# Kernel tuning notes

Hardware: AMD Instinct MI355X
Metric: run time of the kernel (lower is better)

## Reference

```python
import jax, jax.numpy as jnp
import numpy as np

B, N, NY = 2, 4096, 4096
ENC_DIM, DEC_DIM, H = 768, 512, 8
HEAD_DIM = DEC_DIM // H
SCALE = HEAD_DIM ** -0.5


def setup_inputs() -> dict:
    key = jax.random.key(0)
    ks = jax.random.split(key, 8)
    lim_q = 1.0 / np.sqrt(DEC_DIM)
    lim_kv = 1.0 / np.sqrt(ENC_DIM)
    return {
        "x": jax.random.normal(ks[0], (B, N, DEC_DIM), jnp.float32),
        "y": jax.random.normal(ks[1], (B, NY, ENC_DIM), jnp.float32),
        "key_padding_mask": jax.random.randint(ks[2], (B, NY), 0, 2).astype(bool),
        "Wq": jax.random.uniform(ks[3], (DEC_DIM, DEC_DIM), jnp.float32, -lim_q, lim_q),
        "Wkv": jax.random.uniform(ks[4], (2 * DEC_DIM, ENC_DIM), jnp.float32, -lim_kv, lim_kv),
        "Wp": jax.random.uniform(ks[5], (DEC_DIM, DEC_DIM), jnp.float32, -lim_q, lim_q),
        "bp": jax.random.uniform(ks[6], (DEC_DIM,), jnp.float32, -lim_q, lim_q),
    }


def reference(x, y, key_padding_mask, Wq, Wkv, Wp, bp):
    # q projection: [B,N,C] -> [B,H,N,D]
    q = (x @ Wq.T).reshape(B, N, H, HEAD_DIM).transpose(0, 2, 1, 3)
    # kv projection: [B,Ny,E] -> [B,Ny,2C] -> k,v each [B,H,Ny,D]
    kv = (y @ Wkv.T).reshape(B, NY, 2, H, HEAD_DIM).transpose(2, 0, 3, 1, 4)
    k, v = kv[0], kv[1]
    # attention scores [B,H,N,Ny]
    attn = jnp.einsum("bhnd,bhmd->bhnm", q, k) * SCALE
    attn = jnp.where(key_padding_mask[:, None, None, :], -jnp.inf, attn)
    attn = jax.nn.softmax(attn, axis=-1)
    out = jnp.einsum("bhnm,bhmd->bhnd", attn, v)  # [B,H,N,D]
    out = out.transpose(0, 2, 1, 3).reshape(B, N, DEC_DIM)
    return out @ Wp.T + bp
```

## Files before the change

### kernel.cpp

```cpp
#include <hip/hip_runtime.h>
#include <hip/hip_bf16.h>
#include <stdint.h>

typedef __bf16 bf16_t;
typedef __bf16 bf16x8 __attribute__((ext_vector_type(8)));
typedef __bf16 bf16x4 __attribute__((ext_vector_type(4)));
typedef float  f32x4  __attribute__((ext_vector_type(4)));

#define MFMA16(a, b, c) __builtin_amdgcn_mfma_f32_16x16x32_bf16((a), (b), (c), 0, 0, 0)

__device__ __forceinline__ void gload_lds16(const void* g, void* l) {
  __builtin_amdgcn_global_load_lds((const __attribute__((address_space(1))) void*)g,
                                   (__attribute__((address_space(3))) void*)l, 16, 0, 0);
}

#define QSCALE 0.18033688011112042f
#define NE_X   4194304UL
#define NE_Y   6291456UL
#define NE_WQ  262144UL
#define NE_WKV 786432UL
#define NE_WP  262144UL
#define NE_BP  512UL

__global__ void detect_and_mask(const uint16_t* __restrict__ xu,
                                const uint8_t* __restrict__ mk,
                                int* __restrict__ flags, bf16_t* __restrict__ mmul) {
  __shared__ int cbf, c3f1, c3f3, cnz;
  const int t = threadIdx.x;
  if (t == 0) { cbf = 0; c3f1 = 0; c3f3 = 0; cnz = 0; }
  __syncthreads();
  if (blockIdx.x == 0) {
    int local = 0;
    for (int i = t; i < 2048; i += 256) {
      uint16_t u = xu[2 * i];
      int e = (u >> 7) & 0xFF;
      if (u == 0 || (e >= 0x66 && e <= 0x88)) local++;
    }
    atomicAdd(&cbf, local);
  }
  int l1 = 0, l3 = 0, lnz = 0;
  for (int i = t; i < 4096; i += 256) {
    uint8_t b = mk[i];
    int p = i & 3;
    if (p == 1 && b == 0x3F) l1++;
    if (p == 3 && b == 0x3F) l3++;
    if (p != 0 && b != 0) lnz++;
  }
  atomicAdd(&c3f1, l1);
  atomicAdd(&c3f3, l3);
  atomicAdd(&cnz, lnz);
  __syncthreads();
  if (blockIdx.x == 0 && t == 0) flags[0] = (cbf > 1536) ? 1 : 0;
  const int fmt = (c3f1 > 0) ? 2 : (c3f3 > 0) ? 3 : (cnz > 0) ? 0 : 1;
  const int i = blockIdx.x * 256 + t;
  bool on;
  if (fmt == 0)      on = mk[i] != 0;
  else if (fmt == 1) on = ((const int*)mk)[i] != 0;
  else if (fmt == 2) on = (((const uint16_t*)mk)[i] & 0x7FFF) != 0;
  else               on = ((const float*)mk)[i] != 0.0f;
  mmul[i] = on ? (bf16_t)0.0f : (bf16_t)1.0f;
}

__global__ void convert_all(const void* __restrict__ x, const void* __restrict__ y,
                            const void* __restrict__ wq, const void* __restrict__ wkv,
                            const void* __restrict__ wp, const void* __restrict__ bp,
                            uint16_t* __restrict__ dst, const int* __restrict__ flags) {
  const size_t E0 = NE_X, E1 = E0 + NE_Y, E2 = E1 + NE_WQ, E3 = E2 + NE_WKV,
               E4 = E3 + NE_WP, E5 = E4 + NE_BP;
  size_t i8 = ((size_t)blockIdx.x * 256 + threadIdx.x) * 8;
  if (i8 >= E5) return;
  const void* src; size_t off;
  if      (i8 < E0) { src = x;   off = i8; }
  else if (i8 < E1) { src = y;   off = i8 - E0; }
  else if (i8 < E2) { src = wq;  off = i8 - E1; }
  else if (i8 < E3) { src = wkv; off = i8 - E2; }
  else if (i8 < E4) { src = wp;  off = i8 - E3; }
  else              { src = bp;  off = i8 - E4; }
  const bool isWq = (i8 >= E1 && i8 < E2);
  if (flags[0] && !isWq) {
    *(uint4*)(dst + i8) = *(const uint4*)((const uint16_t*)src + off);
    return;
  }
  float v[8];
  if (flags[0]) {
    const uint16_t* u = (const uint16_t*)src + off;
    for (int j = 0; j < 8; ++j) {
      union { uint32_t q; float f; } c; c.q = ((uint32_t)u[j]) << 16; v[j] = c.f;
    }
  } else {
    const float* f = (const float*)src + off;
    float4 a = *(const float4*)f;
    float4 b2 = *(const float4*)(f + 4);
    v[0] = a.x; v[1] = a.y; v[2] = a.z; v[3] = a.w;
    v[4] = b2.x; v[5] = b2.y; v[6] = b2.z; v[7] = b2.w;
  }
  const float sc = isWq ? QSCALE : 1.0f;
  union { bf16_t h[8]; uint4 u; } pk;
  for (int j = 0; j < 8; ++j) pk.h[j] = (bf16_t)(v[j] * sc);
  *(uint4*)(dst + i8) = pk.u;
}

template <int K, int MODE>
__launch_bounds__(256, 2)
__global__ void gemm_bt(const bf16_t* __restrict__ A, const bf16_t* __restrict__ W,
                        const bf16_t* __restrict__ bias, void* __restrict__ C,
                        bf16_t* __restrict__ Vt, const int* __restrict__ flags, int Ncols) {
  __shared__ __align__(16) char lds[16384];
  char* ldsA = lds;
  char* ldsW = lds + 8192;
  const int t = threadIdx.x;
  const int w = t >> 6, lane = t & 63, quad = lane >> 4, l16 = lane & 15;
  const int wr = w >> 1, wc = w & 1;
  const int m0 = blockIdx.y * 128, n0 = blockIdx.x * 128;

  f32x4 acc[4][4] = {};
  const int rowS = t >> 2, uS = t & 3;

  for (int k0 = 0; k0 < K; k0 += 32) {
    __syncthreads();
    for (int i = 0; i < 2; ++i) {
      int row = i * 64 + rowS;
      int c = uS ^ ((row >> 1) & 3);
      gload_lds16(A + (size_t)(m0 + row) * K + k0 + c * 8, ldsA + i * 4096 + w * 1024);
      gload_lds16(W + (size_t)(n0 + row) * K + k0 + c * 8, ldsW + i * 4096 + w * 1024);
    }
    __syncthreads();
    bf16x8 af[4], bfr[4];
    for (int mt = 0; mt < 4; ++mt) {
      int row = wr * 64 + mt * 16 + l16;
      int us = quad ^ ((row >> 1) & 3);
      af[mt] = *(const bf16x8*)(ldsA + row * 64 + us * 16);
    }
    for (int nt = 0; nt < 4; ++nt) {
      int row = wc * 64 + nt * 16 + l16;
      int us = quad ^ ((row >> 1) & 3);
      bfr[nt] = *(const bf16x8*)(ldsW + row * 64 + us * 16);
    }
    for (int mt = 0; mt < 4; ++mt)
      for (int nt = 0; nt < 4; ++nt)
        acc[mt][nt] = MFMA16(af[mt], bfr[nt], acc[mt][nt]);
  }

  const int mbase = m0 + wr * 64;
  for (int nt = 0; nt < 4; ++nt) {
    const int col = n0 + wc * 64 + nt * 16 + l16;
    if (MODE == 1 && col >= 512) {
      const int hd = col - 512;
      const int hh = hd >> 6, d = hd & 63;
      const int dt = d >> 4, l15 = d & 15;
      for (int mt = 0; mt < 4; ++mt) {
        int m = mbase + mt * 16 + quad * 4;
        int bb = m >> 12, keyg = m & 4095;
        int kt = keyg >> 6, keyin = keyg & 63;
        int kc = (keyin >> 5) & 1, jq = (keyin >> 3) & 3, j0 = keyin & 7;
        const bf16_t* mmp = bias + bb * 4096 + keyg;
        union { bf16_t h4[4]; uint2 u; } pk;
        for (int r = 0; r < 4; ++r) pk.h4[r] = (bf16_t)(acc[mt][nt][r] * (float)mmp[r]);
        size_t base = (((size_t)(bb * 8 + hh) * 64 + kt) * 8 + dt * 2 + kc) * 1024
                      + (jq * 16 + l15) * 16 + j0 * 2;
        *(uint2*)((char*)Vt + base) = pk.u;
      }
    } else if (MODE == 1) {
      for (int mt = 0; mt < 4; ++mt) {
        int m = mbase + mt * 16 + quad * 4;
        for (int r = 0; r < 4; ++r)
          ((bf16_t*)C)[(size_t)(m + r) * 512 + col] = (bf16_t)acc[mt][nt][r];
      }
    } else if (MODE == 0) {
      for (int mt = 0; mt < 4; ++mt) {
        int m = mbase + mt * 16 + quad * 4;
        for (int r = 0; r < 4; ++r)
          ((bf16_t*)C)[(size_t)(m + r) * Ncols + col] = (bf16_t)acc[mt][nt][r];
      }
    } else {
      const float bv = (float)bias[col];
      const bool obf = (flags[0] != 0);
      for (int mt = 0; mt < 4; ++mt) {
        int m = mbase + mt * 16 + quad * 4;
        for (int r = 0; r < 4; ++r) {
          float v = acc[mt][nt][r] + bv;
          if (obf) ((bf16_t*)C)[(size_t)(m + r) * Ncols + col] = (bf16_t)v;
          else     ((float*)C)[(size_t)(m + r) * Ncols + col] = v;
        }
      }
    }
  }
}

__launch_bounds__(256, 2)
__global__ void attn(const bf16_t* __restrict__ Qb, const bf16_t* __restrict__ Kb,
                     const bf16_t* __restrict__ Vfb, const bf16_t* __restrict__ mmul,
                     bf16_t* __restrict__ Ob) {
  const int t = threadIdx.x, w = t >> 6, lane = t & 63, quad = lane >> 4, l16 = lane & 15;
  const int q0 = blockIdx.x * 128, h = blockIdx.y, b = blockIdx.z;

  __shared__ __align__(16) char lds[32768];
  char* Pw = lds + 16384 + w * 4096;
  char* Qs = lds + 16384;

  for (int i = 0; i < 4; ++i) {
    int row = i * 32 + (t >> 3);
    int c = (t & 7) ^ (row & 7);
    gload_lds16(Qb + (size_t)(b * 4096 + q0 + row) * 512 + h * 64 + c * 8,
                Qs + i * 4096 + w * 1024);
  }
  for (int i = 0; i < 2; ++i) {
    int row = i * 32 + (t >> 3);
    int c = (t & 7) ^ (row & 7);
    gload_lds16(Kb + (size_t)(b * 4096 + row) * 512 + h * 64 + c * 8,
                lds + i * 4096 + w * 1024);
  }
  __syncthreads();

  bf16x8 qf[2][2];
  for (int ng = 0; ng < 2; ++ng)
    for (int kc = 0; kc < 2; ++kc) {
      int row = 32 * w + 16 * ng + l16;
      int u = (4 * kc + quad) ^ (row & 7);
      qf[ng][kc] = *(const bf16x8*)(Qs + row * 128 + u * 16);
    }
  __syncthreads();

  f32x4 o[2][4] = {};
  f32x4 lacc[2] = {};
  const char* Vfbase = (const char*)Vfb + (size_t)(b * 8 + h) * 524288;

  for (int kt = 0; kt < 64; ++kt) {
    const int cur = kt & 1;
    const int kt0 = kt * 64;
    if (kt + 1 < 64) {
      const int nxt = cur ^ 1;
      for (int i = 0; i < 2; ++i) {
        int row = i * 32 + (t >> 3);
        int c = (t & 7) ^ (row & 7);
        gload_lds16(Kb + (size_t)(b * 4096 + kt0 + 64 + row) * 512 + h * 64 + c * 8,
                    lds + nxt * 8192 + i * 4096 + w * 1024);
      }
    }
    const char* Kl = lds + cur * 8192;

    bf16x8 mf[2];
    mf[0] = *(const bf16x8*)(mmul + b * 4096 + kt0 + quad * 8);
    mf[1] = *(const bf16x8*)(mmul + b * 4096 + kt0 + 32 + quad * 8);
    const char* Vtile = Vfbase + (size_t)kt * 8192;
    bf16x8 vf[4][2];
    for (int dt = 0; dt < 4; ++dt)
      for (int kc = 0; kc < 2; ++kc)
        vf[dt][kc] = *(const bf16x8*)(Vtile + (dt * 2 + kc) * 1024 + lane * 16);

    bf16x8 kf[4][2];
    for (int mt = 0; mt < 4; ++mt)
      for (int kc = 0; kc < 2; ++kc) {
        int row = mt * 16 + l16;
        int u = (4 * kc + quad) ^ (row & 7);
        kf[mt][kc] = *(const bf16x8*)(Kl + row * 128 + u * 16);
      }

    for (int ng = 0; ng < 2; ++ng) {
      const int row = 16 * ng + l16;
      for (int mt = 0; mt < 4; ++mt) {
        f32x4 z = {};
        z = MFMA16(kf[mt][0], qf[ng][0], z);
        z = MFMA16(kf[mt][1], qf[ng][1], z);
        bf16x4 pk;
        pk.x = (bf16_t)__builtin_amdgcn_exp2f(z[0]);
        pk.y = (bf16_t)__builtin_amdgcn_exp2f(z[1]);
        pk.z = (bf16_t)__builtin_amdgcn_exp2f(z[2]);
        pk.w = (bf16_t)__builtin_amdgcn_exp2f(z[3]);
        int c2 = (2 * mt + (quad >> 1)) ^ (row & 7);
        *(bf16x4*)(Pw + row * 128 + c2 * 16 + (quad & 1) * 8) = pk;
      }
    }

    bf16x8 pf[2][2];
    for (int ng = 0; ng < 2; ++ng)
      for (int kc = 0; kc < 2; ++kc) {
        int row = 16 * ng + l16;
        int u = (4 * kc + quad) ^ (row & 7);
        pf[ng][kc] = *(const bf16x8*)(Pw + row * 128 + u * 16);
      }
    for (int ng = 0; ng < 2; ++ng) {
      lacc[ng] = MFMA16(pf[ng][0], mf[0], lacc[ng]);
      lacc[ng] = MFMA16(pf[ng][1], mf[1], lacc[ng]);
    }
    for (int dt = 0; dt < 4; ++dt)
      for (int kc = 0; kc < 2; ++kc) {
        o[0][dt] = MFMA16(pf[0][kc], vf[dt][kc], o[0][dt]);
        o[1][dt] = MFMA16(pf[1][kc], vf[dt][kc], o[1][dt]);
      }

    __syncthreads();
  }

  for (int ng = 0; ng < 2; ++ng) {
    float inv[4];
    for (int r = 0; r < 4; ++r) inv[r] = 1.0f / lacc[ng][r];
    for (int dt = 0; dt < 4; ++dt)
      for (int r = 0; r < 4; ++r) {
        int q = q0 + 32 * w + 16 * ng + quad * 4 + r;
        int col = h * 64 + dt * 16 + l16;
        Ob[(size_t)(b * 4096 + q) * 512 + col] = (bf16_t)(o[ng][dt][r] * inv[r]);
      }
  }
}

extern "C" void kernel_launch(void* const* d_in, const int* in_sizes, int n_in,
                              void* d_out, int out_size, void* d_ws, size_t ws_size,
                              hipStream_t stream) {
  const void* x   = d_in[0];
  const void* y   = d_in[1];
  const void* msk = d_in[2];
  const void* Wq  = d_in[3];
  const void* Wkv = d_in[4];
  const void* Wp  = d_in[5];
  const void* bp  = d_in[6];

  char* ws = (char*)d_ws;
  bf16_t* Xb   = (bf16_t*)(ws + 0);
  bf16_t* Yb   = (bf16_t*)(ws + 8388608);
  bf16_t* Wqb  = (bf16_t*)(ws + 20971520);
  bf16_t* Wkvb = (bf16_t*)(ws + 21495808);
  bf16_t* Wpb  = (bf16_t*)(ws + 23068672);
  bf16_t* bpb  = (bf16_t*)(ws + 23592960);
  bf16_t* mmul = (bf16_t*)(ws + 23593984);
  int*    flags = (int*)(ws + 23610368);
  bf16_t* Kbuf  = (bf16_t*)(ws + 25165824);
  bf16_t* Vfrag = (bf16_t*)(ws + 33554432);
  bf16_t* Qbuf  = (bf16_t*)(ws + 8388608);
  bf16_t* Obuf  = (bf16_t*)(ws + 0);

  hipLaunchKernelGGL(detect_and_mask, dim3(32), dim3(256), 0, stream,
                     (const uint16_t*)x, (const uint8_t*)msk, flags, mmul);
  hipLaunchKernelGGL(convert_all, dim3(5761), dim3(256), 0, stream,
                     x, y, Wq, Wkv, Wp, bp, (uint16_t*)ws, flags);
  hipLaunchKernelGGL((gemm_bt<768, 1>), dim3(8, 64), dim3(256), 0, stream,
                     Yb, Wkvb, mmul, (void*)Kbuf, Vfrag, flags, 1024);
  hipLaunchKernelGGL((gemm_bt<512, 0>), dim3(4, 64), dim3(256), 0, stream,
                     Xb, Wqb, (const bf16_t*)nullptr, (void*)Qbuf, (bf16_t*)nullptr, flags, 512);
  hipLaunchKernelGGL(attn, dim3(32, 8, 2), dim3(256), 0, stream,
                     Qbuf, Kbuf, Vfrag, mmul, Obuf);
  hipLaunchKernelGGL((gemm_bt<512, 2>), dim3(4, 64), dim3(256), 0, stream,
                     Obuf, Wpb, bpb, d_out, (bf16_t*)nullptr, flags, 512);
}
```

Before: 269.7 us.

## Process two K tiles per barrier with a 4-slot K ring and MFMA priority

The attention kernel now keeps a 4-slot LDS ring of K tiles. It prefetches two tiles ahead and handles two 64-key tiles between each __syncthreads, which halves the number of block barriers. QK^T results are collected into a register array before the exp step, and the MFMA sections are wrapped in s_setprio raises so matrix work is favoured over other waves. The 3D grid is flattened to 1D with head as the fastest index, which changes block scheduling order. The cost is 48KB of LDS per block, which could limit occupancy, and extra register pressure from the unrolled pair loop.

Measured after the change: 238.2 us. 11.7% less time.

```diff
diff --git a/kernel.cpp b/kernel.cpp
--- a/kernel.cpp
+++ b/kernel.cpp
@@ -192,11 +192,14 @@
                      const bf16_t* __restrict__ Vfb, const bf16_t* __restrict__ mmul,
                      bf16_t* __restrict__ Ob) {
   const int t = threadIdx.x, w = t >> 6, lane = t & 63, quad = lane >> 4, l16 = lane & 15;
-  const int q0 = blockIdx.x * 128, h = blockIdx.y, b = blockIdx.z;
-
-  __shared__ __align__(16) char lds[32768];
-  char* Pw = lds + 16384 + w * 4096;
-  char* Qs = lds + 16384;
+  const int bid = blockIdx.x;
+  const int h = bid & 7;
+  const int b = (bid >> 3) & 1;
+  const int q0 = (bid >> 4) * 128;
+
+  __shared__ __align__(16) char lds[49152];
+  char* Pw = lds + 32768 + w * 4096;
+  char* Qs = lds + 32768;
 
   for (int i = 0; i < 4; ++i) {
     int row = i * 32 + (t >> 3);
@@ -204,12 +207,13 @@
     gload_lds16(Qb + (size_t)(b * 4096 + q0 + row) * 512 + h * 64 + c * 8,
                 Qs + i * 4096 + w * 1024);
   }
-  for (int i = 0; i < 2; ++i) {
-    int row = i * 32 + (t >> 3);
-    int c = (t & 7) ^ (row & 7);
-    gload_lds16(Kb + (size_t)(b * 4096 + row) * 512 + h * 64 + c * 8,
-                lds + i * 4096 + w * 1024);
-  }
+  for (int kt = 0; kt < 2; ++kt)
+    for (int i = 0; i < 2; ++i) {
+      int row = i * 32 + (t >> 3);
+      int c = (t & 7) ^ (row & 7);
+      gload_lds16(Kb + (size_t)(b * 4096 + kt * 64 + row) * 512 + h * 64 + c * 8,
+                  lds + kt * 8192 + i * 4096 + w * 1024);
+    }
   __syncthreads();
 
   bf16x8 qf[2][2];
@@ -225,70 +229,84 @@
   f32x4 lacc[2] = {};
   const char* Vfbase = (const char*)Vfb + (size_t)(b * 8 + h) * 524288;
 
-  for (int kt = 0; kt < 64; ++kt) {
-    const int cur = kt & 1;
-    const int kt0 = kt * 64;
-    if (kt + 1 < 64) {
-      const int nxt = cur ^ 1;
-      for (int i = 0; i < 2; ++i) {
-        int row = i * 32 + (t >> 3);
-        int c = (t & 7) ^ (row & 7);
-        gload_lds16(Kb + (size_t)(b * 4096 + kt0 + 64 + row) * 512 + h * 64 + c * 8,
-                    lds + nxt * 8192 + i * 4096 + w * 1024);
-      }
-    }
-    const char* Kl = lds + cur * 8192;
-
-    bf16x8 mf[2];
-    mf[0] = *(const bf16x8*)(mmul + b * 4096 + kt0 + quad * 8);
-    mf[1] = *(const bf16x8*)(mmul + b * 4096 + kt0 + 32 + quad * 8);
-    const char* Vtile = Vfbase + (size_t)kt * 8192;
-    bf16x8 vf[4][2];
-    for (int dt = 0; dt < 4; ++dt)
-      for (int kc = 0; kc < 2; ++kc)
-        vf[dt][kc] = *(const bf16x8*)(Vtile + (dt * 2 + kc) * 1024 + lane * 16);
-
-    bf16x8 kf[4][2];
-    for (int mt = 0; mt < 4; ++mt)
-      for (int kc = 0; kc < 2; ++kc) {
-        int row = mt * 16 + l16;
-        int u = (4 * kc + quad) ^ (row & 7);
-        kf[mt][kc] = *(const bf16x8*)(Kl + row * 128 + u * 16);
-      }
-
-    for (int ng = 0; ng < 2; ++ng) {
-      const int row = 16 * ng + l16;
-      for (int mt = 0; mt < 4; ++mt) {
-        f32x4 z = {};
-        z = MFMA16(kf[mt][0], qf[ng][0], z);
-        z = MFMA16(kf[mt][1], qf[ng][1], z);
-        bf16x4 pk;
-        pk.x = (bf16_t)__builtin_amdgcn_exp2f(z[0]);
-        pk.y = (bf16_t)__builtin_amdgcn_exp2f(z[1]);
-        pk.z = (bf16_t)__builtin_amdgcn_exp2f(z[2]);
-        pk.w = (bf16_t)__builtin_amdgcn_exp2f(z[3]);
-        int c2 = (2 * mt + (quad >> 1)) ^ (row & 7);
-        *(bf16x4*)(Pw + row * 128 + c2 * 16 + (quad & 1) * 8) = pk;
-      }
-    }
-
-    bf16x8 pf[2][2];
-    for (int ng = 0; ng < 2; ++ng)
-      for (int kc = 0; kc < 2; ++kc) {
-        int row = 16 * ng + l16;
-        int u = (4 * kc + quad) ^ (row & 7);
-        pf[ng][kc] = *(const bf16x8*)(Pw + row * 128 + u * 16);
-      }
-    for (int ng = 0; ng < 2; ++ng) {
-      lacc[ng] = MFMA16(pf[ng][0], mf[0], lacc[ng]);
-      lacc[ng] = MFMA16(pf[ng][1], mf[1], lacc[ng]);
-    }
-    for (int dt = 0; dt < 4; ++dt)
-      for (int kc = 0; kc < 2; ++kc) {
-        o[0][dt] = MFMA16(pf[0][kc], vf[dt][kc], o[0][dt]);
-        o[1][dt] = MFMA16(pf[1][kc], vf[dt][kc], o[1][dt]);
-      }
-
+  for (int ktp = 0; ktp < 32; ++ktp) {
+    const int ktA = ktp * 2;
+    if (ktp + 1 < 32) {
+      for (int kk = 2; kk < 4; ++kk) {
+        const int kt = ktA + kk;
+        for (int i = 0; i < 2; ++i) {
+          int row = i * 32 + (t >> 3);
+          int c = (t & 7) ^ (row & 7);
+          gload_lds16(Kb + (size_t)(b * 4096 + kt * 64 + row) * 512 + h * 64 + c * 8,
+                      lds + (kt & 3) * 8192 + i * 4096 + w * 1024);
+        }
+      }
+    }
+#pragma unroll
+    for (int kk = 0; kk < 2; ++kk) {
+      const int kt = ktA + kk;
+      const int kt0 = kt * 64;
+      const char* Kl = lds + (kt & 3) * 8192;
+
+      bf16x8 mf[2];
+      mf[0] = *(const bf16x8*)(mmul + b * 4096 + kt0 + quad * 8);
+      mf[1] = *(const bf16x8*)(mmul + b * 4096 + kt0 + 32 + quad * 8);
+      const char* Vtile = Vfbase + (size_t)kt * 8192;
+      bf16x8 vf[4][2];
+      for (int dt = 0; dt < 4; ++dt)
+        for (int kc = 0; kc < 2; ++kc)
+          vf[dt][kc] = *(const bf16x8*)(Vtile + (dt * 2 + kc) * 1024 + lane * 16);
+
+      bf16x8 kf[4][2];
+      for (int mt = 0; mt < 4; ++mt)
+        for (int kc = 0; kc < 2; ++kc) {
+          int row = mt * 16 + l16;
+          int u = (4 * kc + quad) ^ (row & 7);
+          kf[mt][kc] = *(const bf16x8*)(Kl + row * 128 + u * 16);
+        }
+
+      f32x4 z[2][4];
+      __builtin_amdgcn_s_setprio(1);
+      for (int ng = 0; ng < 2; ++ng)
+        for (int mt = 0; mt < 4; ++mt) {
+          f32x4 zz = {};
+          zz = MFMA16(kf[mt][0], qf[ng][0], zz);
+          z[ng][mt] = MFMA16(kf[mt][1], qf[ng][1], zz);
+        }
+      __builtin_amdgcn_s_setprio(0);
+
+      for (int ng = 0; ng < 2; ++ng) {
+        const int row = 16 * ng + l16;
+        for (int mt = 0; mt < 4; ++mt) {
+          bf16x4 pk;
+          pk.x = (bf16_t)__builtin_amdgcn_exp2f(z[ng][mt][0]);
+          pk.y = (bf16_t)__builtin_amdgcn_exp2f(z[ng][mt][1]);
+          pk.z = (bf16_t)__builtin_amdgcn_exp2f(z[ng][mt][2]);
+          pk.w = (bf16_t)__builtin_amdgcn_exp2f(z[ng][mt][3]);
+          int c2 = (2 * mt + (quad >> 1)) ^ (row & 7);
+          *(bf16x4*)(Pw + row * 128 + c2 * 16 + (quad & 1) * 8) = pk;
+        }
+      }
+
+      bf16x8 pf[2][2];
+      for (int ng = 0; ng < 2; ++ng)
+        for (int kc = 0; kc < 2; ++kc) {
+          int row = 16 * ng + l16;
+          int u = (4 * kc + quad) ^ (row & 7);
+          pf[ng][kc] = *(const bf16x8*)(Pw + row * 128 + u * 16);
+        }
+      __builtin_amdgcn_s_setprio(1);
+      for (int ng = 0; ng < 2; ++ng) {
+        lacc[ng] = MFMA16(pf[ng][0], mf[0], lacc[ng]);
+        lacc[ng] = MFMA16(pf[ng][1], mf[1], lacc[ng]);
+      }
+      for (int dt = 0; dt < 4; ++dt)
+        for (int kc = 0; kc < 2; ++kc) {
+          o[0][dt] = MFMA16(pf[0][kc], vf[dt][kc], o[0][dt]);
+          o[1][dt] = MFMA16(pf[1][kc], vf[dt][kc], o[1][dt]);
+        }
+      __builtin_amdgcn_s_setprio(0);
+    }
     __syncthreads();
   }
 
@@ -337,7 +355,7 @@
                      Yb, Wkvb, mmul, (void*)Kbuf, Vfrag, flags, 1024);
   hipLaunchKernelGGL((gemm_bt<512, 0>), dim3(4, 64), dim3(256), 0, stream,
                      Xb, Wqb, (const bf16_t*)nullptr, (void*)Qbuf, (bf16_t*)nullptr, flags, 512);
-  hipLaunchKernelGGL(attn, dim3(32, 8, 2), dim3(256), 0, stream,
+  hipLaunchKernelGGL(attn, dim3(512), dim3(256), 0, stream,
                      Qbuf, Kbuf, Vfrag, mmul, Obuf);
   hipLaunchKernelGGL((gemm_bt<512, 2>), dim3(4, 64), dim3(256), 0, stream,
                      Obuf, Wpb, bpb, d_out, (bf16_t*)nullptr, flags, 512);
```
